# Kernel optimization log

Measured on AMD Instinct MI355X. Metric: run time of the kernel, lower is better.

## Reference

```python
import jax, jax.numpy as jnp
import numpy as np

# Key observation: the TF module groups ROIs per image (boolean_mask), runs the
# same MLP on each group, concatenates the ragged results, then argsort-gathers
# to restore the ORIGINAL row order. Since the Dense/ReLU MLP acts row-wise and
# identically for every image, the group -> MLP -> regroup pipeline is exactly
# equivalent to applying the MLP to all rows in their original order. The clean
# JAX reference therefore computes the same math with a single fused GEMM chain.

NUM_CLASSES = 81
HIDDEN_DIM = 1024
N = 2048          # total ROIs
SS = 7            # sample_size
FS = 256          # feature_size
FEAT_DIM = SS * SS * FS  # 12544
NUM_IMAGES = 8


def setup_inputs() -> dict:
    key = jax.random.key(0)
    ks = jax.random.split(key, 8)
    features = jax.random.normal(ks[0], (N, SS, SS, FS), dtype=jnp.float32)
    batch_indices = jnp.sort(jax.random.randint(ks[1], (N,), 0, NUM_IMAGES, dtype=jnp.int32))
    s1 = 1.0 / np.sqrt(FEAT_DIM)
    s2 = 1.0 / np.sqrt(HIDDEN_DIM)
    W1 = jax.random.uniform(ks[2], (FEAT_DIM, HIDDEN_DIM), jnp.float32, -s1, s1)
    b1 = jnp.zeros((HIDDEN_DIM,), jnp.float32)
    W2 = jax.random.uniform(ks[3], (HIDDEN_DIM, HIDDEN_DIM), jnp.float32, -s2, s2)
    b2 = jnp.zeros((HIDDEN_DIM,), jnp.float32)
    Wc = jax.random.uniform(ks[4], (HIDDEN_DIM, NUM_CLASSES), jnp.float32, -s2, s2)
    bc = jnp.zeros((NUM_CLASSES,), jnp.float32)
    return {"features": features, "batch_indices": batch_indices,
            "W1": W1, "b1": b1, "W2": W2, "b2": b2, "Wc": Wc, "bc": bc}


def reference(features, batch_indices, W1, b1, W2, b2, Wc, bc):
    # Group/ungroup in the original is an identity permutation on rows, but we
    # reproduce it explicitly and cheaply: stable-sort rows by image id, run the
    # MLP, then invert the permutation via argsort (same as TF argsort-gather).
    order = jnp.argsort(batch_indices, stable=True)          # group rows per image
    x = features[order].reshape(features.shape[0], -1)       # [N, feat_dim]
    x = jax.nn.relu(x @ W1 + b1)
    x = jax.nn.relu(x @ W2 + b2)
    logits = x @ Wc + bc                                     # [N, num_classes]
    inv = jnp.argsort(order)                                 # restore original order
    return logits[inv]
```

## Files before the change

### kernel.cpp

```cpp
#include <hip/hip_runtime.h>
#include <hip/hip_bf16.h>
#include <stdint.h>

typedef __bf16 bf16_t;
typedef __bf16 bf16x4 __attribute__((ext_vector_type(4)));
typedef __bf16 bf16x8 __attribute__((ext_vector_type(8)));
typedef float f32x4 __attribute__((ext_vector_type(4)));

#define BM 128
#define BN 128
#define BK 32

__device__ __forceinline__ void async_ld16(const bf16_t* g, bf16_t* lds) {
    __builtin_amdgcn_global_load_lds(
        (__attribute__((address_space(1))) void*)g,
        (__attribute__((address_space(3))) void*)lds,
        16, 0, 0);
}


__device__ __forceinline__ void transpose_tile(
    const float* __restrict__ in, bf16_t* __restrict__ out,
    int R, int C, int Cp, int tileIdx, int tid, float (*tile)[33])
{
    const int tilesX = Cp / 32;
    const int c0 = (tileIdx % tilesX) * 32;
    const int r0 = (tileIdx / tilesX) * 32;
    const int tx = tid & 31;
    const int ty = tid >> 5;
#pragma unroll
    for (int i = 0; i < 32; i += 8) {
        int rr = r0 + ty + i, cc = c0 + tx;
        float v = 0.f;
        if (cc < C) v = in[(size_t)rr * C + cc];
        tile[ty + i][tx] = v;
    }
    __syncthreads();
#pragma unroll
    for (int i = 0; i < 32; i += 8) {
        int oc = c0 + ty + i;
        int orr = r0 + tx;
        out[(size_t)oc * R + orr] = (bf16_t)tile[tx][ty + i];
    }
}

__global__ void prep_all(const float* __restrict__ X, bf16_t* __restrict__ Xb, int n4,
                         const float* __restrict__ W1, bf16_t* __restrict__ W1T,
                         const float* __restrict__ W2, bf16_t* __restrict__ W2T,
                         const float* __restrict__ Wc, bf16_t* __restrict__ WcT,
                         int FEAT, int HID, int NC, int NCP,
                         int nCvt, int t1, int t2)
{
    __shared__ float tile[32][33];
    int bid = blockIdx.x;
    int tid = threadIdx.x;
    if (bid < nCvt) {
        int i = bid * 256 + tid;
        if (i < n4) {
            float4 v = ((const float4*)X)[i];
            bf16x4 o = { (bf16_t)v.x, (bf16_t)v.y, (bf16_t)v.z, (bf16_t)v.w };
            ((bf16x4*)Xb)[i] = o;
        }
        return;
    }
    bid -= nCvt;
    if (bid < t1) { transpose_tile(W1, W1T, FEAT, HID, HID, bid, tid, tile); return; }
    bid -= t1;
    if (bid < t2) { transpose_tile(W2, W2T, HID, HID, HID, bid, tid, tile); return; }
    bid -= t2;
    transpose_tile(Wc, WcT, HID, NC, NCP, bid, tid, tile);
}

__global__ __launch_bounds__(256) void gemm_bf16(
    const bf16_t* __restrict__ A, const bf16_t* __restrict__ B,
    float* __restrict__ P, int M, int N, int K, int Kchunk)
{
    __shared__ __align__(16) bf16_t Asm[BM * BK];
    __shared__ __align__(16) bf16_t Bsm[BN * BK];

    const int tid  = threadIdx.x;
    const int wave = tid >> 6;
    const int lane = tid & 63;
    const int bm = blockIdx.x, bn = blockIdx.y, s = blockIdx.z;

    const bf16_t* Ab = A + (size_t)bm * BM * K + (size_t)s * Kchunk;
    const bf16_t* Bb = B + (size_t)bn * BN * K + (size_t)s * Kchunk;

    const int ar = lane >> 2;
    const int ak = (lane & 3) * 8;

    const int wm = (wave >> 1) * 64;
    const int wn = (wave & 1) * 64;
    const int kq = (lane >> 4) * 8;
    const int r  = lane & 15;

    f32x4 acc[4][4];
#pragma unroll
    for (int i = 0; i < 4; ++i)
#pragma unroll
        for (int j = 0; j < 4; ++j)
            acc[i][j] = f32x4{0.f, 0.f, 0.f, 0.f};

    for (int k0 = 0; k0 < Kchunk; k0 += BK) {
        __syncthreads();
#pragma unroll
        for (int i = 0; i < 2; ++i) {
            const int rb = (wave * 2 + i) * 16;
            async_ld16(Ab + (size_t)(rb + ar) * K + (k0 + ak), &Asm[rb * BK]);
            async_ld16(Bb + (size_t)(rb + ar) * K + (k0 + ak), &Bsm[rb * BK]);
        }
        __syncthreads();

        bf16x8 af[4], bfr[4];
#pragma unroll
        for (int i = 0; i < 4; ++i)
            af[i] = *(const bf16x8*)&Asm[(wm + i * 16 + r) * BK + kq];
#pragma unroll
        for (int j = 0; j < 4; ++j)
            bfr[j] = *(const bf16x8*)&Bsm[(wn + j * 16 + r) * BK + kq];
#pragma unroll
        for (int i = 0; i < 4; ++i)
#pragma unroll
            for (int j = 0; j < 4; ++j)
                acc[i][j] = __builtin_amdgcn_mfma_f32_16x16x32_bf16(af[i], bfr[j], acc[i][j], 0, 0, 0);
    }

    float* Pb = P + ((size_t)s * M + (size_t)bm * BM) * N + (size_t)bn * BN;
    const int r4 = (lane >> 4) * 4;
    const int c  = lane & 15;
#pragma unroll
    for (int i = 0; i < 4; ++i)
#pragma unroll
        for (int j = 0; j < 4; ++j)
#pragma unroll
            for (int rg = 0; rg < 4; ++rg)
                Pb[(size_t)(wm + i * 16 + r4 + rg) * N + (wn + j * 16 + c)] = acc[i][j][rg];
}


template <int S>
__global__ void reduce_relu_bf16_k(const float* __restrict__ P, const float* __restrict__ bias,
                                   bf16_t* __restrict__ h, int MN, int Nm1) {
    int i4 = (blockIdx.x * 256 + threadIdx.x) * 4;
    if (i4 >= MN) return;
    int n = i4 & Nm1;
    float4 a = *(const float4*)(bias + n);
#pragma unroll
    for (int s = 0; s < S; ++s) {
        float4 p = *(const float4*)(P + (size_t)s * MN + i4);
        a.x += p.x; a.y += p.y; a.z += p.z; a.w += p.w;
    }
    a.x = fmaxf(a.x, 0.f); a.y = fmaxf(a.y, 0.f);
    a.z = fmaxf(a.z, 0.f); a.w = fmaxf(a.w, 0.f);
    bf16x4 o = { (bf16_t)a.x, (bf16_t)a.y, (bf16_t)a.z, (bf16_t)a.w };
    *(bf16x4*)(h + i4) = o;
}

template <int S>
__global__ void reduce_out_k(const float* __restrict__ P, const float* __restrict__ bc,
                             float* __restrict__ out, int M, int NC, int NCP) {
    int idx = blockIdx.x * 256 + threadIdx.x;
    if (idx >= M * NC) return;
    int m = idx / NC;
    int n = idx - m * NC;
    float a = bc[n];
    size_t MN = (size_t)M * NCP;
#pragma unroll
    for (int s = 0; s < S; ++s)
        a += P[s * MN + (size_t)m * NCP + n];
    out[idx] = a;
}


extern "C" void kernel_launch(void* const* d_in, const int* in_sizes, int n_in,
                              void* d_out, int out_size, void* d_ws, size_t ws_size,
                              hipStream_t stream) {
    const float* X  = (const float*)d_in[0];
    const float* W1 = (const float*)d_in[2];
    const float* b1 = (const float*)d_in[3];
    const float* W2 = (const float*)d_in[4];
    const float* b2 = (const float*)d_in[5];
    const float* Wc = (const float*)d_in[6];
    const float* bc = (const float*)d_in[7];
    float* out = (float*)d_out;

    const int M    = in_sizes[1];
    const int FEAT = in_sizes[0] / M;
    const int HID  = in_sizes[3];
    const int NC   = in_sizes[7];
    const int NCP  = 128;

    char* ws = (char*)d_ws;
    size_t off = 0;
    auto alloc = [&](size_t bytes) {
        char* p = ws + off;
        off += (bytes + 255) & ~(size_t)255;
        return p;
    };
    bf16_t* Xb  = (bf16_t*)alloc((size_t)M * FEAT * 2);
    bf16_t* W1T = (bf16_t*)alloc((size_t)FEAT * HID * 2);
    bf16_t* W2T = (bf16_t*)alloc((size_t)HID * HID * 2);
    bf16_t* WcT = (bf16_t*)alloc((size_t)NCP * HID * 2);
    bf16_t* h1  = (bf16_t*)alloc((size_t)M * HID * 2);
    bf16_t* h2  = (bf16_t*)alloc((size_t)M * HID * 2);
    float*  P   = (float*)(ws + off);

    size_t rem  = ws_size > off ? ws_size - off : 0;
    size_t perS = (size_t)M * HID * 4;
    int S1 = (rem >= 8 * perS) ? 8 : (rem >= 4 * perS) ? 4 : (rem >= 2 * perS) ? 2 : 1;
    int S2 = (S1 >= 4) ? 4 : S1;
    const int S3 = 8;

    int n4   = (M * FEAT) / 4;
    int nCvt = (n4 + 255) / 256;
    int t1 = (HID / 32) * (FEAT / 32);
    int t2 = (HID / 32) * (HID / 32);
    int t3 = (NCP / 32) * (HID / 32);
    prep_all<<<nCvt + t1 + t2 + t3, 256, 0, stream>>>(
        X, Xb, n4, W1, W1T, W2, W2T, Wc, WcT, FEAT, HID, NC, NCP, nCvt, t1, t2);

    gemm_bf16<<<dim3(M / BM, HID / BN, S1), 256, 0, stream>>>(Xb, W1T, P, M, HID, FEAT, FEAT / S1);
    switch (S1) {
        case 8: reduce_relu_bf16_k<8><<<(M * HID / 4 + 255) / 256, 256, 0, stream>>>(P, b1, h1, M * HID, HID - 1); break;
        case 4: reduce_relu_bf16_k<4><<<(M * HID / 4 + 255) / 256, 256, 0, stream>>>(P, b1, h1, M * HID, HID - 1); break;
        case 2: reduce_relu_bf16_k<2><<<(M * HID / 4 + 255) / 256, 256, 0, stream>>>(P, b1, h1, M * HID, HID - 1); break;
        default: reduce_relu_bf16_k<1><<<(M * HID / 4 + 255) / 256, 256, 0, stream>>>(P, b1, h1, M * HID, HID - 1); break;
    }

    gemm_bf16<<<dim3(M / BM, HID / BN, S2), 256, 0, stream>>>(h1, W2T, P, M, HID, HID, HID / S2);
    switch (S2) {
        case 4: reduce_relu_bf16_k<4><<<(M * HID / 4 + 255) / 256, 256, 0, stream>>>(P, b2, h2, M * HID, HID - 1); break;
        case 2: reduce_relu_bf16_k<2><<<(M * HID / 4 + 255) / 256, 256, 0, stream>>>(P, b2, h2, M * HID, HID - 1); break;
        default: reduce_relu_bf16_k<1><<<(M * HID / 4 + 255) / 256, 256, 0, stream>>>(P, b2, h2, M * HID, HID - 1); break;
    }

    gemm_bf16<<<dim3(M / BM, NCP / BN, S3), 256, 0, stream>>>(h2, WcT, P, M, NCP, HID, HID / S3);
    reduce_out_k<S3><<<(M * NC + 255) / 256, 256, 0, stream>>>(P, bc, out, M, NC, NCP);
}
```

Baseline: 323.8 us.

## Deepen GEMM K-step to 64 and fuse bias/ReLU epilogue into non-split GEMMs

The first split-K GEMM now stages 64-wide K tiles in LDS and runs two MFMA rounds per barrier pair, halving synchronisation per unit of work. The second and third GEMMs drop split-K and the separate reduction kernels, using a new 64x64-tile kernel that applies bias, optional ReLU and the output cast directly in its epilogue. This removes the large fp32 partial-sum traffic and two extra launches, at the cost of less K-parallelism and smaller tiles with lower reuse for the later layers.

Measured after the change: 324.8 us. No clear change (+0.3%).

```diff
diff --git a/kernel.cpp b/kernel.cpp
--- a/kernel.cpp
+++ b/kernel.cpp
@@ -6,10 +6,6 @@
 typedef __bf16 bf16x4 __attribute__((ext_vector_type(4)));
 typedef __bf16 bf16x8 __attribute__((ext_vector_type(8)));
 typedef float f32x4 __attribute__((ext_vector_type(4)));
-
-#define BM 128
-#define BN 128
-#define BK 32
 
 __device__ __forceinline__ void async_ld16(const bf16_t* g, bf16_t* lds) {
     __builtin_amdgcn_global_load_lds(
@@ -71,23 +67,26 @@
     transpose_tile(Wc, WcT, HID, NC, NCP, bid, tid, tile);
 }
 
-__global__ __launch_bounds__(256) void gemm_bf16(
+__global__ __launch_bounds__(256) void gemm128_splitk(
     const bf16_t* __restrict__ A, const bf16_t* __restrict__ B,
-    float* __restrict__ P, int M, int N, int K, int Kchunk)
+    float* __restrict__ P, int M, int N, int K, int KC)
 {
-    __shared__ __align__(16) bf16_t Asm[BM * BK];
-    __shared__ __align__(16) bf16_t Bsm[BN * BK];
+    __shared__ __align__(16) bf16_t Asm[128 * 64];
+    __shared__ __align__(16) bf16_t Bsm[128 * 64];
 
     const int tid  = threadIdx.x;
     const int wave = tid >> 6;
     const int lane = tid & 63;
     const int bm = blockIdx.x, bn = blockIdx.y, s = blockIdx.z;
 
-    const bf16_t* Ab = A + (size_t)bm * BM * K + (size_t)s * Kchunk;
-    const bf16_t* Bb = B + (size_t)bn * BN * K + (size_t)s * Kchunk;
-
-    const int ar = lane >> 2;
-    const int ak = (lane & 3) * 8;
+    const int Koff = s * KC;
+    const int Kc   = (K - Koff < KC) ? (K - Koff) : KC;
+
+    const bf16_t* Ab = A + (size_t)bm * 128 * K + Koff;
+    const bf16_t* Bb = B + (size_t)bn * 128 * K + Koff;
+
+    const int sr = lane >> 3;
+    const int sk = (lane & 7) * 8;
 
     const int wm = (wave >> 1) * 64;
     const int wn = (wave & 1) * 64;
@@ -101,31 +100,35 @@
         for (int j = 0; j < 4; ++j)
             acc[i][j] = f32x4{0.f, 0.f, 0.f, 0.f};
 
-    for (int k0 = 0; k0 < Kchunk; k0 += BK) {
+    for (int k0 = 0; k0 < Kc; k0 += 64) {
         __syncthreads();
 #pragma unroll
-        for (int i = 0; i < 2; ++i) {
-            const int rb = (wave * 2 + i) * 16;
-            async_ld16(Ab + (size_t)(rb + ar) * K + (k0 + ak), &Asm[rb * BK]);
-            async_ld16(Bb + (size_t)(rb + ar) * K + (k0 + ak), &Bsm[rb * BK]);
+        for (int i = 0; i < 4; ++i) {
+            const int rb = wave * 32 + i * 8;
+            async_ld16(Ab + (size_t)(rb + sr) * K + (k0 + sk), &Asm[rb * 64]);
+            async_ld16(Bb + (size_t)(rb + sr) * K + (k0 + sk), &Bsm[rb * 64]);
         }
         __syncthreads();
 
-        bf16x8 af[4], bfr[4];
-#pragma unroll
-        for (int i = 0; i < 4; ++i)
-            af[i] = *(const bf16x8*)&Asm[(wm + i * 16 + r) * BK + kq];
-#pragma unroll
-        for (int j = 0; j < 4; ++j)
-            bfr[j] = *(const bf16x8*)&Bsm[(wn + j * 16 + r) * BK + kq];
-#pragma unroll
-        for (int i = 0; i < 4; ++i)
+#pragma unroll
+        for (int rnd = 0; rnd < 2; ++rnd) {
+            const int kb = rnd * 32 + kq;
+            bf16x8 af[4], bfr[4];
+#pragma unroll
+            for (int i = 0; i < 4; ++i)
+                af[i] = *(const bf16x8*)&Asm[(wm + i * 16 + r) * 64 + kb];
 #pragma unroll
             for (int j = 0; j < 4; ++j)
-                acc[i][j] = __builtin_amdgcn_mfma_f32_16x16x32_bf16(af[i], bfr[j], acc[i][j], 0, 0, 0);
-    }
-
-    float* Pb = P + ((size_t)s * M + (size_t)bm * BM) * N + (size_t)bn * BN;
+                bfr[j] = *(const bf16x8*)&Bsm[(wn + j * 16 + r) * 64 + kb];
+#pragma unroll
+            for (int i = 0; i < 4; ++i)
+#pragma unroll
+                for (int j = 0; j < 4; ++j)
+                    acc[i][j] = __builtin_amdgcn_mfma_f32_16x16x32_bf16(af[i], bfr[j], acc[i][j], 0, 0, 0);
+        }
+    }
+
+    float* Pb = P + ((size_t)s * M + (size_t)bm * 128) * N + (size_t)bn * 128;
     const int r4 = (lane >> 4) * 4;
     const int c  = lane & 15;
 #pragma unroll
@@ -135,6 +138,86 @@
 #pragma unroll
             for (int rg = 0; rg < 4; ++rg)
                 Pb[(size_t)(wm + i * 16 + r4 + rg) * N + (wn + j * 16 + c)] = acc[i][j][rg];
+}
+
+template <bool RELU, typename OutT>
+__global__ __launch_bounds__(256) void gemm64_fused(
+    const bf16_t* __restrict__ A, const bf16_t* __restrict__ B,
+    const float* __restrict__ bias, OutT* __restrict__ out,
+    int K, int Nout)
+{
+    __shared__ __align__(16) bf16_t Asm[64 * 64];
+    __shared__ __align__(16) bf16_t Bsm[64 * 64];
+
+    const int tid  = threadIdx.x;
+    const int wave = tid >> 6;
+    const int lane = tid & 63;
+    const int bm = blockIdx.x, bn = blockIdx.y;
+
+    const bf16_t* Ab = A + (size_t)bm * 64 * K;
+    const bf16_t* Bb = B + (size_t)bn * 64 * K;
+
+    const int sr = lane >> 3;
+    const int sk = (lane & 7) * 8;
+
+    const int wm = (wave >> 1) * 32;
+    const int wn = (wave & 1) * 32;
+    const int kq = (lane >> 4) * 8;
+    const int r  = lane & 15;
+
+    f32x4 acc[2][2];
+#pragma unroll
+    for (int i = 0; i < 2; ++i)
+#pragma unroll
+        for (int j = 0; j < 2; ++j)
+            acc[i][j] = f32x4{0.f, 0.f, 0.f, 0.f};
+
+    for (int k0 = 0; k0 < K; k0 += 64) {
+        __syncthreads();
+#pragma unroll
+        for (int i = 0; i < 2; ++i) {
+            const int rb = wave * 16 + i * 8;
+            async_ld16(Ab + (size_t)(rb + sr) * K + (k0 + sk), &Asm[rb * 64]);
+            async_ld16(Bb + (size_t)(rb + sr) * K + (k0 + sk), &Bsm[rb * 64]);
+        }
+        __syncthreads();
+
+#pragma unroll
+        for (int rnd = 0; rnd < 2; ++rnd) {
+            const int kb = rnd * 32 + kq;
+            bf16x8 af[2], bfr[2];
+#pragma unroll
+            for (int i = 0; i < 2; ++i)
+                af[i] = *(const bf16x8*)&Asm[(wm + i * 16 + r) * 64 + kb];
+#pragma unroll
+            for (int j = 0; j < 2; ++j)
+                bfr[j] = *(const bf16x8*)&Bsm[(wn + j * 16 + r) * 64 + kb];
+#pragma unroll
+            for (int i = 0; i < 2; ++i)
+#pragma unroll
+                for (int j = 0; j < 2; ++j)
+                    acc[i][j] = __builtin_amdgcn_mfma_f32_16x16x32_bf16(af[i], bfr[j], acc[i][j], 0, 0, 0);
+        }
+    }
+
+    const int r4 = (lane >> 4) * 4;
+    const int c  = lane & 15;
+#pragma unroll
+    for (int i = 0; i < 2; ++i)
+#pragma unroll
+        for (int j = 0; j < 2; ++j) {
+            const int col = bn * 64 + wn + j * 16 + c;
+            if (col < Nout) {
+                const float bv = bias[col];
+#pragma unroll
+                for (int rg = 0; rg < 4; ++rg) {
+                    const int row = bm * 64 + wm + i * 16 + r4 + rg;
+                    float v = acc[i][j][rg] + bv;
+                    if (RELU) v = fmaxf(v, 0.f);
+                    out[(size_t)row * Nout + col] = (OutT)v;
+                }
+            }
+        }
 }
 
 
@@ -154,21 +237,6 @@
     a.z = fmaxf(a.z, 0.f); a.w = fmaxf(a.w, 0.f);
     bf16x4 o = { (bf16_t)a.x, (bf16_t)a.y, (bf16_t)a.z, (bf16_t)a.w };
     *(bf16x4*)(h + i4) = o;
-}
-
-template <int S>
-__global__ void reduce_out_k(const float* __restrict__ P, const float* __restrict__ bc,
-                             float* __restrict__ out, int M, int NC, int NCP) {
-    int idx = blockIdx.x * 256 + threadIdx.x;
-    if (idx >= M * NC) return;
-    int m = idx / NC;
-    int n = idx - m * NC;
-    float a = bc[n];
-    size_t MN = (size_t)M * NCP;
-#pragma unroll
-    for (int s = 0; s < S; ++s)
-        a += P[s * MN + (size_t)m * NCP + n];
-    out[idx] = a;
 }
 
 
@@ -208,8 +276,7 @@
     size_t rem  = ws_size > off ? ws_size - off : 0;
     size_t perS = (size_t)M * HID * 4;
     int S1 = (rem >= 8 * perS) ? 8 : (rem >= 4 * perS) ? 4 : (rem >= 2 * perS) ? 2 : 1;
-    int S2 = (S1 >= 4) ? 4 : S1;
-    const int S3 = 8;
+    int KC1 = ((FEAT / S1 + 63) / 64) * 64;
 
     int n4   = (M * FEAT) / 4;
     int nCvt = (n4 + 255) / 256;
@@ -219,7 +286,7 @@
     prep_all<<<nCvt + t1 + t2 + t3, 256, 0, stream>>>(
         X, Xb, n4, W1, W1T, W2, W2T, Wc, WcT, FEAT, HID, NC, NCP, nCvt, t1, t2);
 
-    gemm_bf16<<<dim3(M / BM, HID / BN, S1), 256, 0, stream>>>(Xb, W1T, P, M, HID, FEAT, FEAT / S1);
+    gemm128_splitk<<<dim3(M / 128, HID / 128, S1), 256, 0, stream>>>(Xb, W1T, P, M, HID, FEAT, KC1);
     switch (S1) {
         case 8: reduce_relu_bf16_k<8><<<(M * HID / 4 + 255) / 256, 256, 0, stream>>>(P, b1, h1, M * HID, HID - 1); break;
         case 4: reduce_relu_bf16_k<4><<<(M * HID / 4 + 255) / 256, 256, 0, stream>>>(P, b1, h1, M * HID, HID - 1); break;
@@ -227,13 +294,7 @@
         default: reduce_relu_bf16_k<1><<<(M * HID / 4 + 255) / 256, 256, 0, stream>>>(P, b1, h1, M * HID, HID - 1); break;
     }
 
-    gemm_bf16<<<dim3(M / BM, HID / BN, S2), 256, 0, stream>>>(h1, W2T, P, M, HID, HID, HID / S2);
-    switch (S2) {
-        case 4: reduce_relu_bf16_k<4><<<(M * HID / 4 + 255) / 256, 256, 0, stream>>>(P, b2, h2, M * HID, HID - 1); break;
-        case 2: reduce_relu_bf16_k<2><<<(M * HID / 4 + 255) / 256, 256, 0, stream>>>(P, b2, h2, M * HID, HID - 1); break;
-        default: reduce_relu_bf16_k<1><<<(M * HID / 4 + 255) / 256, 256, 0, stream>>>(P, b2, h2, M * HID, HID - 1); break;
-    }
-
-    gemm_bf16<<<dim3(M / BM, NCP / BN, S3), 256, 0, stream>>>(h2, WcT, P, M, NCP, HID, HID / S3);
-    reduce_out_k<S3><<<(M * NC + 255) / 256, 256, 0, stream>>>(P, bc, out, M, NC, NCP);
-}
+    gemm64_fused<true, bf16_t><<<dim3(M / 64, HID / 64), 256, 0, stream>>>(h1, W2T, b2, h2, HID, HID);
+
+    gemm64_fused<false, float><<<dim3(M / 64, NCP / 64), 256, 0, stream>>>(h2, WcT, bc, out, HID, NC);
+}
```
